# Optimization experiments

Hardware: AMD Instinct MI355X
Metric: run time of the kernel (lower is better)

Reference implementation:

```python
import jax, jax.numpy as jnp
import numpy as np

B, S, D = 2, 2048, 1024
H = 16
DH = D // H  # 64


def setup_inputs() -> dict:
    key = jax.random.key(0)
    k1, k2, k3, k4, k5 = jax.random.split(key, 5)
    scale = 1.0 / np.sqrt(D)
    return {
        "x": jax.random.normal(k1, (B, S, D), dtype=jnp.float32),
        "w_in": jax.random.normal(k2, (3 * D, D), dtype=jnp.float32) * scale,
        "b_in": jax.random.normal(k3, (3 * D,), dtype=jnp.float32) * 0.02,
        "w_out": jax.random.normal(k4, (D, D), dtype=jnp.float32) * scale,
        "b_out": jax.random.normal(k5, (D,), dtype=jnp.float32) * 0.02,
        "mask": 1,
    }


def reference(x, w_in, b_in, w_out, b_out, mask):
    bs, seq_len, d_emb = x.shape
    # in_proj: torch Linear -> x @ W^T + b
    qkv = jnp.einsum("bsd,ed->bse", x, w_in) + b_in  # (B, S, 3D)
    q, k, v = jnp.split(qkv, 3, axis=-1)
    # (B, S, D) -> (B, H, S, DH)
    def heads(t):
        return t.reshape(bs, seq_len, H, DH).transpose(0, 2, 1, 3)
    q, k, v = heads(q), heads(k), heads(v)
    scores = jnp.einsum("bhqd,bhkd->bhqk", q, k)  # (B, H, S, S)
    if mask:
        causal = jnp.triu(jnp.ones((seq_len, seq_len), dtype=bool), k=1)
        scores = jnp.where(causal, -jnp.inf, scores)
    # original divides after masking; -inf / scale is still -inf
    scores = scores / jnp.sqrt(jnp.asarray(DH, dtype=scores.dtype))
    weights = jax.nn.softmax(scores, axis=-1)
    att = jnp.einsum("bhqk,bhkd->bhqd", weights, v)  # (B, H, S, DH)
    att = att.transpose(0, 2, 1, 3).reshape(bs, seq_len, d_emb)
    out = jnp.einsum("bsd,ed->bse", att, w_out) + b_out
    return out
```

## Files before the change

kernel.cpp:

```cpp
#include <hip/hip_runtime.h>
#include <hip/hip_bf16.h>
#include <stdint.h>


typedef __attribute__((ext_vector_type(8))) short bf16x8;
typedef __attribute__((ext_vector_type(4))) float f32x4;
typedef __attribute__((ext_vector_type(16))) float f32x16;
typedef __attribute__((ext_vector_type(4))) unsigned int u32x4;

typedef const __attribute__((address_space(1))) uint32_t* gp1_t;
typedef __attribute__((address_space(3))) uint32_t* lp3_t;

static __device__ __forceinline__ uint32_t cvtpk(float lo, float hi) {
  uint32_t r;
  asm("v_cvt_pk_bf16_f32 %0, %1, %2" : "=v"(r) : "v"(lo), "v"(hi));
  return r;
}
static __device__ __forceinline__ uint16_t f2b(float x) {
  return (uint16_t)cvtpk(x, x);
}
static __device__ __forceinline__ float fexp2(float x) {
  float r;
  asm("v_exp_f32 %0, %1" : "=v"(r) : "v"(x));
  return r;
}

template <int ISSUES>
static __device__ __forceinline__ void stage64(const uint16_t* __restrict__ g, int gstride,
                                               uint8_t* lds, int t) {
#pragma unroll
  for (int i = 0; i < ISSUES; ++i) {
    int p = i * 256 + t;
    int row = p >> 3, c = p & 7;
    const uint16_t* src = g + row * gstride + ((c ^ (row & 7)) << 3);
    __builtin_amdgcn_global_load_lds((gp1_t)src, (lp3_t)(lds + (p & ~63) * 16), 16, 0, 0);
  }
}

static __device__ __forceinline__ bf16x8 ld_frag(const uint8_t* lds, int row, int chunk) {
  return *(const bf16x8*)(lds + row * 128 + (((chunk) ^ (row & 7)) << 4));
}

__global__ __launch_bounds__(256) void cvt3(const float* __restrict__ a,
                                            const float* __restrict__ b,
                                            const float* __restrict__ c,
                                            uint16_t* __restrict__ oa,
                                            uint16_t* __restrict__ ob,
                                            uint16_t* __restrict__ oc) {
  int i = blockIdx.x * 256 + threadIdx.x;
  const float* src;
  uint16_t* dst;
  int j;
  if (i < 1048576)      { src = a; dst = oa; j = i; }
  else if (i < 1835008) { src = b; dst = ob; j = i - 1048576; }
  else                  { src = c; dst = oc; j = i - 1835008; }
  float4 v = ((const float4*)src)[j];
  uint2 o;
  o.x = cvtpk(v.x, v.y);
  o.y = cvtpk(v.z, v.w);
  ((uint2*)dst)[j] = o;
}

__global__ __launch_bounds__(256) void gemm_qkv(const uint16_t* __restrict__ A,
                                                const uint16_t* __restrict__ W,
                                                const float* __restrict__ bias,
                                                uint16_t* __restrict__ Qb,
                                                uint16_t* __restrict__ Kb,
                                                uint16_t* __restrict__ Vt) {
  __shared__ union {
    uint8_t stage[32768];
    uint16_t ot[128][136];
  } sm;
  uint8_t* As = sm.stage;
  uint8_t* Bs = sm.stage + 16384;
  int t = threadIdx.x, l = t & 63, w = t >> 6;
  int m0 = blockIdx.y * 128, n0 = blockIdx.x * 128;
  int wr = (w >> 1) * 64, wc = (w & 1) * 64;
  const f32x4 fz = {0.f, 0.f, 0.f, 0.f};
  f32x4 acc[4][4];
#pragma unroll
  for (int i = 0; i < 4; ++i)
#pragma unroll
    for (int j = 0; j < 4; ++j) acc[i][j] = fz;

  for (int kt = 0; kt < 16; ++kt) {
    __syncthreads();
    stage64<4>(A + m0 * 1024 + kt * 64, 1024, As, t);
    stage64<4>(W + n0 * 1024 + kt * 64, 1024, Bs, t);
    __syncthreads();
#pragma unroll
    for (int ks = 0; ks < 2; ++ks) {
      bf16x8 a[4], b[4];
#pragma unroll
      for (int i = 0; i < 4; ++i) {
        a[i] = ld_frag(As, wr + i * 16 + (l & 15), ks * 4 + (l >> 4));
        b[i] = ld_frag(Bs, wc + i * 16 + (l & 15), ks * 4 + (l >> 4));
      }
#pragma unroll
      for (int i = 0; i < 4; ++i)
#pragma unroll
        for (int j = 0; j < 4; ++j)
          acc[i][j] = __builtin_amdgcn_mfma_f32_16x16x32_bf16(a[i], b[j], acc[i][j], 0, 0, 0);
    }
  }

  __syncthreads();
  const float CSQ = 0.18033688011112042f;
  int sec = n0 >> 10;
#pragma unroll
  for (int j = 0; j < 4; ++j) {
    int col = wc + j * 16 + (l & 15);
    float bv = bias[n0 + col];
#pragma unroll
    for (int i = 0; i < 4; ++i) {
      int rb = wr + i * 16 + ((l >> 4) << 2);
#pragma unroll
      for (int r = 0; r < 4; ++r) {
        int row = rb + r;
        float v = acc[i][j][r] + bv;
        if (sec == 0) v *= CSQ;
        if (sec == 2) {
          int rowp = (row & ~12) | ((row & 4) << 1) | ((row & 8) >> 1);
          sm.ot[col][rowp] = f2b(v);
        } else {
          sm.ot[row][col] = f2b(v);
        }
      }
    }
  }
  __syncthreads();

  int bb0 = m0 >> 11, sbase = m0 & 2047;
  int h0 = (n0 & 1023) >> 6;
  if (sec < 2) {
    uint16_t* dst0 = (sec == 0) ? Qb : Kb;
    int s_loc = t & 127, hh = t >> 7;
    const uint16_t* src = &sm.ot[s_loc][hh * 64];
    uint16_t* dst = dst0 + (((size_t)((bb0 * 16 + h0 + hh) * 2048 + sbase + s_loc)) << 6);
#pragma unroll
    for (int c = 0; c < 8; ++c)
      *(u32x4*)(dst + c * 8) = *(const u32x4*)(src + c * 8);
  } else {
    int re = t >> 1, scc = t & 1;
    int hh = re >> 6, dh = re & 63;
    const uint16_t* src = &sm.ot[re][scc * 64];
    uint16_t* dst = Vt + ((size_t)((bb0 * 16 + h0 + hh) * 64 + dh)) * 2048 + sbase + scc * 64;
#pragma unroll
    for (int c = 0; c < 8; ++c)
      *(u32x4*)(dst + c * 8) = *(const u32x4*)(src + c * 8);
  }
}

__global__ __launch_bounds__(256) void gemm_out(const uint16_t* __restrict__ A,
                                                const uint16_t* __restrict__ W,
                                                const float* __restrict__ bias,
                                                float* __restrict__ out) {
  __shared__ uint8_t sm[32768];
  uint8_t* As = sm;
  uint8_t* Bs = sm + 16384;
  int t = threadIdx.x, l = t & 63, w = t >> 6;
  int m0 = blockIdx.y * 128, n0 = blockIdx.x * 128;
  int wr = (w >> 1) * 64, wc = (w & 1) * 64;
  const f32x4 fz = {0.f, 0.f, 0.f, 0.f};
  f32x4 acc[4][4];
#pragma unroll
  for (int i = 0; i < 4; ++i)
#pragma unroll
    for (int j = 0; j < 4; ++j) acc[i][j] = fz;

  for (int kt = 0; kt < 16; ++kt) {
    __syncthreads();
    stage64<4>(A + m0 * 1024 + kt * 64, 1024, As, t);
    stage64<4>(W + n0 * 1024 + kt * 64, 1024, Bs, t);
    __syncthreads();
#pragma unroll
    for (int ks = 0; ks < 2; ++ks) {
      bf16x8 a[4], b[4];
#pragma unroll
      for (int i = 0; i < 4; ++i) {
        a[i] = ld_frag(As, wr + i * 16 + (l & 15), ks * 4 + (l >> 4));
        b[i] = ld_frag(Bs, wc + i * 16 + (l & 15), ks * 4 + (l >> 4));
      }
#pragma unroll
      for (int i = 0; i < 4; ++i)
#pragma unroll
        for (int j = 0; j < 4; ++j)
          acc[i][j] = __builtin_amdgcn_mfma_f32_16x16x32_bf16(a[i], b[j], acc[i][j], 0, 0, 0);
    }
  }
#pragma unroll
  for (int j = 0; j < 4; ++j) {
    int e = n0 + wc + j * 16 + (l & 15);
    float bv = bias[e];
#pragma unroll
    for (int i = 0; i < 4; ++i) {
      int mb = m0 + wr + i * 16 + ((l >> 4) << 2);
#pragma unroll
      for (int r = 0; r < 4; ++r) {
        int m = mb + r;
        out[m * 1024 + e] = acc[i][j][r] + bv;
      }
    }
  }
}

__global__ __launch_bounds__(512) void attn(const uint16_t* __restrict__ Qb,
                                            const uint16_t* __restrict__ Kb,
                                            const uint16_t* __restrict__ Vt,
                                            uint16_t* __restrict__ Ab,
                                            const int* __restrict__ maskp) {
  __shared__ uint8_t smem[32768];
  int t = threadIdx.x, l = t & 63, w = t >> 6;
  int hi = l >> 5, ql = l & 31;
  int did = (int)blockIdx.x;
  int xcd = did & 7, idx = did >> 3;
  int bh = xcd * 4 + (idx >> 3);
  int p = idx & 7;
  int g = w >> 2, wg = w & 3;
  bool causal = (*maskp != 0);
  int st = g ? p : 15 - p;
  int ntg = causal ? 2 * (st + 1) : 32;
  int nth = causal ? 2 * (16 - p) : 32;
  int q0w = st * 128 + wg * 32;
  int q = q0w + ql;
  int bb = bh >> 4, h = bh & 15;

  const uint16_t* KpB = Kb + ((size_t)bh << 17);
  const uint16_t* VpB = Vt + ((size_t)bh << 17);

  bf16x8 qf[4];
  const uint16_t* Qp = Qb + (((size_t)bh * 2048 + q) << 6) + hi * 8;
#pragma unroll
  for (int ks = 0; ks < 4; ++ks) qf[ks] = *(const bf16x8*)(Qp + ks * 16);

  f32x16 acco[2];
#pragma unroll
  for (int r = 0; r < 16; ++r) { acco[0][r] = 0.f; acco[1][r] = 0.f; }
  float lsum = 0.f;

  stage64<1>(KpB, 64, smem, t);
  stage64<1>(VpB, 2048, smem + 8192, t);

  for (int tt = 0; tt < nth; ++tt) {
    int cur = tt & 1;
    asm volatile("s_waitcnt vmcnt(0)" ::: "memory");
    __syncthreads();
    if (tt + 1 < nth) {
      uint8_t* nb = smem + ((cur ^ 1) << 14);
      stage64<1>(KpB + ((size_t)(tt + 1) << 12), 64, nb, t);
      stage64<1>(VpB + (tt + 1) * 64, 2048, nb + 8192, t);
    }
    if (tt >= ntg || (causal && tt * 64 > q0w + 31)) continue;

    const uint8_t* Ks = smem + (cur << 14);
    const uint8_t* Vs = Ks + 8192;
    bf16x8 kf[2][4], vf[2][4];
#pragma unroll
    for (int ks = 0; ks < 4; ++ks) {
      kf[0][ks] = ld_frag(Ks, ql,      ks * 2 + hi);
      kf[1][ks] = ld_frag(Ks, 32 + ql, ks * 2 + hi);
      vf[0][ks] = ld_frag(Vs, ql,      ks * 2 + hi);
      vf[1][ks] = ld_frag(Vs, 32 + ql, ks * 2 + hi);
    }

    f32x16 sc[2];
#pragma unroll
    for (int r = 0; r < 16; ++r) { sc[0][r] = 0.f; sc[1][r] = 0.f; }
    __builtin_amdgcn_s_setprio(1);
#pragma unroll
    for (int ks = 0; ks < 4; ++ks)
      sc[0] = __builtin_amdgcn_mfma_f32_32x32x16_bf16(kf[0][ks], qf[ks], sc[0], 0, 0, 0);
#pragma unroll
    for (int ks = 0; ks < 4; ++ks)
      sc[1] = __builtin_amdgcn_mfma_f32_32x32x16_bf16(kf[1][ks], qf[ks], sc[1], 0, 0, 0);
    __builtin_amdgcn_s_setprio(0);

    bool nomask = (!causal) || (tt * 64 + 63 <= q0w);
    int qrel = q - tt * 64;
    float rs0 = 0.f, rs1 = 0.f, rs2 = 0.f, rs3 = 0.f;

#pragma unroll
    for (int r = 0; r < 16; ++r) {
      float v = sc[0][r];
      if (!nomask) {
        int kv = (r & 3) + 8 * (r >> 2) + 4 * hi;
        v = (kv <= qrel) ? v : -1e30f;
      }
      float e = fexp2(v);
      sc[0][r] = e;
      if (r & 1) rs1 += e; else rs0 += e;
    }

    __builtin_amdgcn_s_setprio(1);
#pragma unroll
    for (int ks = 0; ks < 2; ++ks) {
      int a8 = ks * 8;
      u32x4 wv = {cvtpk(sc[0][a8 + 0], sc[0][a8 + 1]),
                  cvtpk(sc[0][a8 + 2], sc[0][a8 + 3]),
                  cvtpk(sc[0][a8 + 4], sc[0][a8 + 5]),
                  cvtpk(sc[0][a8 + 6], sc[0][a8 + 7])};
      bf16x8 af = __builtin_bit_cast(bf16x8, wv);
      acco[0] = __builtin_amdgcn_mfma_f32_32x32x16_bf16(af, vf[0][ks], acco[0], 0, 0, 0);
      acco[1] = __builtin_amdgcn_mfma_f32_32x32x16_bf16(af, vf[1][ks], acco[1], 0, 0, 0);
    }
    __builtin_amdgcn_s_setprio(0);

#pragma unroll
    for (int r = 0; r < 16; ++r) {
      float v = sc[1][r];
      if (!nomask) {
        int kv = 32 + (r & 3) + 8 * (r >> 2) + 4 * hi;
        v = (kv <= qrel) ? v : -1e30f;
      }
      float e = fexp2(v);
      sc[1][r] = e;
      if (r & 1) rs3 += e; else rs2 += e;
    }

    __builtin_amdgcn_s_setprio(1);
#pragma unroll
    for (int ks = 0; ks < 2; ++ks) {
      int a8 = ks * 8;
      u32x4 wv = {cvtpk(sc[1][a8 + 0], sc[1][a8 + 1]),
                  cvtpk(sc[1][a8 + 2], sc[1][a8 + 3]),
                  cvtpk(sc[1][a8 + 4], sc[1][a8 + 5]),
                  cvtpk(sc[1][a8 + 6], sc[1][a8 + 7])};
      bf16x8 af = __builtin_bit_cast(bf16x8, wv);
      acco[0] = __builtin_amdgcn_mfma_f32_32x32x16_bf16(af, vf[0][ks + 2], acco[0], 0, 0, 0);
      acco[1] = __builtin_amdgcn_mfma_f32_32x32x16_bf16(af, vf[1][ks + 2], acco[1], 0, 0, 0);
    }
    __builtin_amdgcn_s_setprio(0);

    lsum += (rs0 + rs1) + (rs2 + rs3);
  }

  lsum += __shfl_xor(lsum, 32);
#pragma unroll
  for (int r = 0; r < 16; ++r) {
    int crow = (r & 3) + 8 * (r >> 2) + 4 * hi;
    float L = __shfl(lsum, crow);
    float inv = 1.0f / L;
    int qg = q0w + crow;
#pragma unroll
    for (int n = 0; n < 2; ++n)
      Ab[(((size_t)(bb * 2048 + qg)) << 10) + h * 64 + n * 32 + ql] = f2b(acco[n][r] * inv);
  }
}

extern "C" void kernel_launch(void* const* d_in, const int* in_sizes, int n_in,
                              void* d_out, int out_size, void* d_ws, size_t ws_size,
                              hipStream_t stream) {
  const float* x     = (const float*)d_in[0];
  const float* w_in  = (const float*)d_in[1];
  const float* b_in  = (const float*)d_in[2];
  const float* w_out = (const float*)d_in[3];
  const float* b_out = (const float*)d_in[4];
  const int*   mask  = (const int*)d_in[5];
  float* out = (float*)d_out;

  uint8_t* ws = (uint8_t*)d_ws;
  uint16_t* xb  = (uint16_t*)(ws);
  uint16_t* wib = (uint16_t*)(ws + (8u << 20));
  uint16_t* wob = (uint16_t*)(ws + (14u << 20));
  uint16_t* Qb  = (uint16_t*)(ws + (16u << 20));
  uint16_t* Kb  = (uint16_t*)(ws + (24u << 20));
  uint16_t* Vt  = (uint16_t*)(ws + (32u << 20));
  uint16_t* Ab  = (uint16_t*)(ws + (40u << 20));

  cvt3<<<8192, 256, 0, stream>>>(x, w_in, w_out, xb, wib, wob);
  gemm_qkv<<<dim3(24, 32), 256, 0, stream>>>(xb, wib, b_in, Qb, Kb, Vt);
  attn<<<256, 512, 0, stream>>>(Qb, Kb, Vt, Ab, mask);
  gemm_out<<<dim3(8, 32), 256, 0, stream>>>(Ab, wob, b_out, out);
}
```

Before: 132.4 us.

## Double-buffer LDS staging in QKV and output projection GEMMs

Both projection GEMMs now use two 32KB LDS buffers. The next K-tile's global-to-LDS copy is issued before the MFMA work on the current tile, and one barrier per iteration replaces two. The goal is to hide global load latency behind compute. The cost is double the LDS per block (64KB), which may reduce how many blocks fit on each CU.

```diff
diff --git a/kernel.cpp b/kernel.cpp
--- a/kernel.cpp
+++ b/kernel.cpp
@@ -68,11 +68,9 @@
                                                 uint16_t* __restrict__ Kb,
                                                 uint16_t* __restrict__ Vt) {
   __shared__ union {
-    uint8_t stage[32768];
+    uint8_t stage[65536];
     uint16_t ot[128][136];
   } sm;
-  uint8_t* As = sm.stage;
-  uint8_t* Bs = sm.stage + 16384;
   int t = threadIdx.x, l = t & 63, w = t >> 6;
   int m0 = blockIdx.y * 128, n0 = blockIdx.x * 128;
   int wr = (w >> 1) * 64, wc = (w & 1) * 64;
@@ -83,18 +81,28 @@
 #pragma unroll
     for (int j = 0; j < 4; ++j) acc[i][j] = fz;
 
+  const uint16_t* Ab_ = A + m0 * 1024;
+  const uint16_t* Wb_ = W + n0 * 1024;
+  stage64<4>(Ab_, 1024, sm.stage, t);
+  stage64<4>(Wb_, 1024, sm.stage + 16384, t);
+
   for (int kt = 0; kt < 16; ++kt) {
+    int cur = kt & 1;
+    uint8_t* curb = sm.stage + (cur << 15);
+    asm volatile("s_waitcnt vmcnt(0)" ::: "memory");
     __syncthreads();
-    stage64<4>(A + m0 * 1024 + kt * 64, 1024, As, t);
-    stage64<4>(W + n0 * 1024 + kt * 64, 1024, Bs, t);
-    __syncthreads();
+    if (kt + 1 < 16) {
+      uint8_t* nb = sm.stage + ((cur ^ 1) << 15);
+      stage64<4>(Ab_ + (kt + 1) * 64, 1024, nb, t);
+      stage64<4>(Wb_ + (kt + 1) * 64, 1024, nb + 16384, t);
+    }
 #pragma unroll
     for (int ks = 0; ks < 2; ++ks) {
       bf16x8 a[4], b[4];
 #pragma unroll
       for (int i = 0; i < 4; ++i) {
-        a[i] = ld_frag(As, wr + i * 16 + (l & 15), ks * 4 + (l >> 4));
-        b[i] = ld_frag(Bs, wc + i * 16 + (l & 15), ks * 4 + (l >> 4));
+        a[i] = ld_frag(curb, wr + i * 16 + (l & 15), ks * 4 + (l >> 4));
+        b[i] = ld_frag(curb + 16384, wc + i * 16 + (l & 15), ks * 4 + (l >> 4));
       }
 #pragma unroll
       for (int i = 0; i < 4; ++i)
@@ -155,9 +163,7 @@
                                                 const uint16_t* __restrict__ W,
                                                 const float* __restrict__ bias,
                                                 float* __restrict__ out) {
-  __shared__ uint8_t sm[32768];
-  uint8_t* As = sm;
-  uint8_t* Bs = sm + 16384;
+  __shared__ uint8_t sm[65536];
   int t = threadIdx.x, l = t & 63, w = t >> 6;
   int m0 = blockIdx.y * 128, n0 = blockIdx.x * 128;
   int wr = (w >> 1) * 64, wc = (w & 1) * 64;
@@ -168,18 +174,28 @@
 #pragma unroll
     for (int j = 0; j < 4; ++j) acc[i][j] = fz;
 
+  const uint16_t* Ab_ = A + m0 * 1024;
+  const uint16_t* Wb_ = W + n0 * 1024;
+  stage64<4>(Ab_, 1024, sm, t);
+  stage64<4>(Wb_, 1024, sm + 16384, t);
+
   for (int kt = 0; kt < 16; ++kt) {
+    int cur = kt & 1;
+    uint8_t* curb = sm + (cur << 15);
+    asm volatile("s_waitcnt vmcnt(0)" ::: "memory");
     __syncthreads();
-    stage64<4>(A + m0 * 1024 + kt * 64, 1024, As, t);
-    stage64<4>(W + n0 * 1024 + kt * 64, 1024, Bs, t);
-    __syncthreads();
+    if (kt + 1 < 16) {
+      uint8_t* nb = sm + ((cur ^ 1) << 15);
+      stage64<4>(Ab_ + (kt + 1) * 64, 1024, nb, t);
+      stage64<4>(Wb_ + (kt + 1) * 64, 1024, nb + 16384, t);
+    }
 #pragma unroll
     for (int ks = 0; ks < 2; ++ks) {
       bf16x8 a[4], b[4];
 #pragma unroll
       for (int i = 0; i < 4; ++i) {
-        a[i] = ld_frag(As, wr + i * 16 + (l & 15), ks * 4 + (l >> 4));
-        b[i] = ld_frag(Bs, wc + i * 16 + (l & 15), ks * 4 + (l >> 4));
+        a[i] = ld_frag(curb, wr + i * 16 + (l & 15), ks * 4 + (l >> 4));
+        b[i] = ld_frag(curb + 16384, wc + i * 16 + (l & 15), ks * 4 + (l >> 4));
       }
 #pragma unroll
       for (int i = 0; i < 4; ++i)
```

Result: faster. 124.8 us (-5.7%).
